# Kernel tuning notes

Measured on AMD Instinct MI355X. Metric: run time of the kernel, lower is better.

Reference implementation:

```python
import jax, jax.numpy as jnp
import numpy as np

WIRES = 4
DIM = 16  # 2**WIRES
EPS = 1e-5


def _rot_matrix(phi, theta, omega):
    # PennyLane Rot = RZ(omega) RY(theta) RZ(phi)
    c = jnp.cos(theta / 2).astype(jnp.complex64)
    s = jnp.sin(theta / 2).astype(jnp.complex64)
    ep = jnp.exp(-0.5j * (phi + omega).astype(jnp.complex64))
    em = jnp.exp(0.5j * (phi - omega).astype(jnp.complex64))
    m00 = ep * c
    m01 = -em * s
    m10 = jnp.conj(em) * s
    m11 = jnp.conj(ep) * c
    return jnp.stack([jnp.stack([m00, m01]), jnp.stack([m10, m11])])


def _apply_1q(state4, U, w):
    # state4: (B,2,2,2,2); apply 2x2 unitary on wire w (axis w+1)
    st = jnp.moveaxis(state4, w + 1, -1)
    st = st @ U.T  # sum_j st[...,j] * U[i,j]
    return jnp.moveaxis(st, -1, w + 1)


def _cnot_perm(c, t):
    # permutation of 16 basis indices for CNOT(control=c, target=t); wire 0 = MSB
    idx = np.arange(DIM)
    cbit = (idx >> (WIRES - 1 - c)) & 1
    return idx ^ (cbit << (WIRES - 1 - t))


def _circuit(x16, params):
    # AmplitudeEmbedding with normalize=True
    B = x16.shape[0]
    nrm = jnp.linalg.norm(x16, axis=1, keepdims=True)
    state = (x16 / nrm).astype(jnp.complex64)  # (B,16)
    L = params.shape[0]
    for l in range(L):
        st4 = state.reshape(B, 2, 2, 2, 2)
        for w in range(WIRES):
            U = _rot_matrix(params[l, w, 0], params[l, w, 1], params[l, w, 2])
            st4 = _apply_1q(st4, U, w)
        state = st4.reshape(B, DIM)
        r = (l % (WIRES - 1)) + 1  # StronglyEntanglingLayers default range
        for w in range(WIRES):
            perm = _cnot_perm(w, (w + r) % WIRES)
            state = state[:, perm]
    probs = (state.real ** 2 + state.imag ** 2)  # (B,16)
    p4 = probs.reshape(B, 2, 2, 2, 2)
    # <Z_w> = P(bit_w=0) - P(bit_w=1)
    outs = []
    for w in range(WIRES):
        axes = tuple(a for a in range(1, 5) if a != w + 1)
        pw = p4.sum(axis=axes)  # (B,2)
        outs.append(pw[:, 0] - pw[:, 1])
    return jnp.stack(outs, axis=1)  # (B,4)


def setup_inputs() -> dict:
    key = jax.random.key(0)
    k1, k2 = jax.random.split(key)
    B = 65536
    x = jax.random.normal(k1, (B, 1, 24, 24), dtype=jnp.float32)
    params = jax.random.normal(k2, (2, WIRES, 3), dtype=jnp.float32)
    gamma = jnp.ones((WIRES,), dtype=jnp.float32)
    beta = jnp.zeros((WIRES,), dtype=jnp.float32)
    return {"x": x, "params": params, "gamma": gamma, "beta": beta}


def reference(x, params, gamma, beta):
    B = x.shape[0]
    # avg_pool2d kernel 6: (B,1,24,24) -> (B,1,4,4) -> (B,16)
    pooled = x.reshape(B, 1, 4, 6, 4, 6).mean(axis=(3, 5)).reshape(B, DIM)
    out = _circuit(pooled, params)  # (B,4)
    # BatchNorm1d in training mode (biased batch stats)
    mu = out.mean(axis=0)
    var = ((out - mu) ** 2).mean(axis=0)
    return (out - mu) / jnp.sqrt(var + EPS) * gamma + beta
```

## Files before the change

kernel.cpp:

```cpp
#include <hip/hip_runtime.h>
#include <math.h>

#define BATCH 65536
#define XPER  576
#define NBLK  1024
#define WPB   4
#define RPW   2
#define IPR   8


__global__ __launch_bounds__(256, 3) void circuit_kernel(
        const float* __restrict__ x, const float* __restrict__ params,
        float* __restrict__ out, float* __restrict__ slots) {
    __shared__ float sUr[16 * 20];
    __shared__ float sUi[16 * 20];
    __shared__ float sg[48];
    __shared__ float sv[WPB][IPR * 20];
    __shared__ float spart[8];

    const int t    = threadIdx.x;
    const int wid  = t >> 6;
    const int lane = t & 63;
    const int e    = lane >> 3;
    const int q    = lane & 7;
    const int pr   = q >> 1;
    const int P    = q & 1;

    if (t < 8) {
        spart[t] = 0.0f;
        float phi   = params[t * 3 + 0];
        float theta = params[t * 3 + 1];
        float omega = params[t * 3 + 2];
        float apo = 0.5f * (phi + omega), amo = 0.5f * (phi - omega);
        sg[t * 6 + 0] = cosf(0.5f * theta);
        sg[t * 6 + 1] = sinf(0.5f * theta);
        sg[t * 6 + 2] = cosf(apo);
        sg[t * 6 + 3] = -sinf(apo);
        sg[t * 6 + 4] = cosf(amo);
        sg[t * 6 + 5] = sinf(amo);
    }
    __syncthreads();

    if (t < 16) {
        const int j = t;
        float Mr[16], Mi[16];
#pragma unroll
        for (int i = 0; i < 16; ++i) { Mr[i] = (i == j) ? 1.0f : 0.0f; Mi[i] = 0.0f; }
#pragma unroll
        for (int l = 0; l < 2; ++l) {
#pragma unroll
            for (int w = 0; w < 4; ++w) {
                const int g = l * 4 + w;
                float c   = sg[g * 6 + 0], s   = sg[g * 6 + 1];
                float epr = sg[g * 6 + 2], epi = sg[g * 6 + 3];
                float emr = sg[g * 6 + 4], emi = sg[g * 6 + 5];
                float m00r =  epr * c, m00i =  epi * c;
                float m01r = -emr * s, m01i = -emi * s;
                float m10r =  emr * s, m10i = -emi * s;
                float m11r =  epr * c, m11i = -epi * c;
                const int mask = 1 << (3 - w);
#pragma unroll
                for (int i = 0; i < 16; ++i) {
                    if (i & mask) continue;
                    int i1 = i | mask;
                    float r0 = Mr[i],  q0 = Mi[i];
                    float r1 = Mr[i1], q1 = Mi[i1];
                    Mr[i]  = m00r * r0 - m00i * q0 + m01r * r1 - m01i * q1;
                    Mi[i]  = m00r * q0 + m00i * r0 + m01r * q1 + m01i * r1;
                    Mr[i1] = m10r * r0 - m10i * q0 + m11r * r1 - m11i * q1;
                    Mi[i1] = m10r * q0 + m10i * r0 + m11r * q1 + m11i * r1;
                }
            }
            const int rr = (l % 3) + 1;
#pragma unroll
            for (int w = 0; w < 4; ++w) {
                int tq = (w + rr) & 3;
                int cb = 3 - w, tb = 3 - tq;
#pragma unroll
                for (int i = 0; i < 16; ++i) {
                    int pi = i ^ (((i >> cb) & 1) << tb);
                    if (pi > i) {
                        float tr = Mr[i]; Mr[i] = Mr[pi]; Mr[pi] = tr;
                        float ti = Mi[i]; Mi[i] = Mi[pi]; Mi[pi] = ti;
                    }
                }
            }
        }
#pragma unroll
        for (int i = 0; i < 16; ++i) {
            sUr[i * 20 + j] = Mr[i];
            sUi[i * 20 + j] = Mi[i];
        }
    }
    __syncthreads();

    float u0r[16], u0i[16], u1r[16], u1i[16];
    {
        const float4* r0 = (const float4*)(sUr + (2 * q) * 20);
        const float4* r1 = (const float4*)(sUr + (2 * q + 1) * 20);
        const float4* i0 = (const float4*)(sUi + (2 * q) * 20);
        const float4* i1 = (const float4*)(sUi + (2 * q + 1) * 20);
#pragma unroll
        for (int m = 0; m < 4; ++m) {
            float4 a = r0[m], b = r1[m], cc = i0[m], d = i1[m];
            u0r[4*m+0]=a.x; u0r[4*m+1]=a.y; u0r[4*m+2]=a.z; u0r[4*m+3]=a.w;
            u1r[4*m+0]=b.x; u1r[4*m+1]=b.y; u1r[4*m+2]=b.z; u1r[4*m+3]=b.w;
            u0i[4*m+0]=cc.x; u0i[4*m+1]=cc.y; u0i[4*m+2]=cc.z; u0i[4*m+3]=cc.w;
            u1i[4*m+0]=d.x; u1i[4*m+1]=d.y; u1i[4*m+2]=d.z; u1i[4*m+3]=d.w;
        }
    }

    int c = -1;
    if      (q == 4) c = 0;
    else if (q == 2) c = 1;
    else if (q == 1) c = 2;
    else if (q == 0) c = 3;

    const int cbase = pr * 144 + P * 12;
    float accz = 0.0f, accz2 = 0.0f;

#pragma unroll
    for (int rd = 0; rd < RPW; ++rd) {
        const size_t img = (size_t)blockIdx.x * 64 + wid * 16 + rd * 8 + e;
        const float* ip = x + img * XPER + cbase;

        float L = 0.0f, R = 0.0f;
#pragma unroll
        for (int r = 0; r < 6; ++r) {
            float4 a = *(const float4*)(ip + r * 24);
            float4 b = *(const float4*)(ip + r * 24 + 4);
            float4 d = *(const float4*)(ip + r * 24 + 8);
            L += a.x + a.y + a.z + a.w + b.x + b.y;
            R += b.z + b.w + d.x + d.y + d.z + d.w;
        }
        float vL = L * (1.0f / 36.0f), vR = R * (1.0f / 36.0f);

        *(float2*)(&sv[wid][e * 20 + 2 * q]) = make_float2(vL, vR);
        float vv[16];
        {
            const float4* vb = (const float4*)(&sv[wid][e * 20]);
#pragma unroll
            for (int m = 0; m < 4; ++m) {
                float4 a = vb[m];
                vv[4*m+0]=a.x; vv[4*m+1]=a.y; vv[4*m+2]=a.z; vv[4*m+3]=a.w;
            }
        }

        float n2 = 0.0f, sr0 = 0.0f, si0 = 0.0f, sr1 = 0.0f, si1 = 0.0f;
#pragma unroll
        for (int j = 0; j < 16; ++j) {
            float vj = vv[j];
            n2  = fmaf(vj, vj, n2);
            sr0 = fmaf(u0r[j], vj, sr0); si0 = fmaf(u0i[j], vj, si0);
            sr1 = fmaf(u1r[j], vj, sr1); si1 = fmaf(u1i[j], vj, si1);
        }
        float inv = 1.0f / n2;
        float p0 = (sr0 * sr0 + si0 * si0) * inv;
        float p1 = (sr1 * sr1 + si1 * si1) * inv;

        float u = p0 + p1, d = p0 - p1, o;
        o = __shfl_xor(u, 1); u = (q & 1) ? (o - u) : (u + o);
        o = __shfl_xor(u, 2); u = (q & 2) ? (o - u) : (u + o);
        o = __shfl_xor(u, 4); u = (q & 4) ? (o - u) : (u + o);
        d += __shfl_xor(d, 1);
        d += __shfl_xor(d, 2);
        d += __shfl_xor(d, 4);

        if (c >= 0) {
            float z = (q == 0) ? d : u;
            out[img * 4 + c] = z;
            accz  += z;
            accz2 += z * z;
        }
    }

    if (c >= 0) {
        atomicAdd(&spart[c], accz);
        atomicAdd(&spart[4 + c], accz2);
    }
    __syncthreads();
    if (t < 8) slots[blockIdx.x * 8 + t] = spart[t];
}

__global__ __launch_bounds__(256) void bn_apply(float* __restrict__ out,
                                                const float* __restrict__ slots,
                                                const float* __restrict__ gamma,
                                                const float* __restrict__ beta) {
    __shared__ float red[256];
    __shared__ float sc[8];
    const int t = threadIdx.x;
    const int ch = t & 7, g = t >> 3;
    float s = 0.0f;
#pragma unroll
    for (int k = 0; k < NBLK / 32; ++k)
        s += slots[(size_t)(g + 32 * k) * 8 + ch];
    red[t] = s;
    __syncthreads();
#pragma unroll
    for (int stp = 128; stp >= 8; stp >>= 1) {
        if (t < stp) red[t] += red[t + stp];
        __syncthreads();
    }
    if (t < 4) {
        float mu  = red[t] * (1.0f / BATCH);
        float var = red[4 + t] * (1.0f / BATCH) - mu * mu;
        float a = gamma[t] * rsqrtf(var + 1e-5f);
        sc[t]     = a;
        sc[4 + t] = beta[t] - mu * a;
    }
    __syncthreads();
    int i = blockIdx.x * 256 + t;
    float4 z = ((float4*)out)[i];
    z.x = fmaf(z.x, sc[0], sc[4]);
    z.y = fmaf(z.y, sc[1], sc[5]);
    z.z = fmaf(z.z, sc[2], sc[6]);
    z.w = fmaf(z.w, sc[3], sc[7]);
    ((float4*)out)[i] = z;
}

extern "C" void kernel_launch(void* const* d_in, const int* in_sizes, int n_in,
                              void* d_out, int out_size, void* d_ws, size_t ws_size,
                              hipStream_t stream) {
    const float* x      = (const float*)d_in[0];
    const float* params = (const float*)d_in[1];
    const float* gamma  = (const float*)d_in[2];
    const float* beta   = (const float*)d_in[3];
    float* out = (float*)d_out;
    float* ws  = (float*)d_ws;

    hipLaunchKernelGGL(circuit_kernel, dim3(NBLK), dim3(256), 0, stream,
                       x, params, out, ws);
    hipLaunchKernelGGL(bn_apply, dim3(BATCH / 256), dim3(256), 0, stream,
                       out, ws, gamma, beta);
}
```

Before: 36.05 us.

## Coalesce image loads across wave and pool via LDS atomics

Each wave now reads its eight images as one contiguous block, with each lane loading consecutive float4s, instead of each lane walking strided rows of its own 6x12 patch. The pooling partial sums are scattered into per-wave LDS accumulators with atomicAdd, using precomputed per-lane bin indices. The unitary rows are read from LDS inside the dot-product loop rather than kept in registers, and the four outputs per image are gathered by shuffle into a single float4 store. The aim is better global-load coalescing and lower register pressure, at the cost of many LDS atomics and extra LDS traffic. The occupancy hint in launch bounds is also dropped.

```diff
diff --git a/kernel.cpp b/kernel.cpp
--- a/kernel.cpp
+++ b/kernel.cpp
@@ -9,13 +9,13 @@
 #define IPR   8
 
 
-__global__ __launch_bounds__(256, 3) void circuit_kernel(
+__global__ __launch_bounds__(256) void circuit_kernel(
         const float* __restrict__ x, const float* __restrict__ params,
         float* __restrict__ out, float* __restrict__ slots) {
     __shared__ float sUr[16 * 20];
     __shared__ float sUi[16 * 20];
     __shared__ float sg[48];
-    __shared__ float sv[WPB][IPR * 20];
+    __shared__ float sacc[WPB][160];
     __shared__ float spart[8];
 
     const int t    = threadIdx.x;
@@ -23,8 +23,6 @@
     const int lane = t & 63;
     const int e    = lane >> 3;
     const int q    = lane & 7;
-    const int pr   = q >> 1;
-    const int P    = q & 1;
 
     if (t < 8) {
         spart[t] = 0.0f;
@@ -94,21 +92,20 @@
     }
     __syncthreads();
 
-    float u0r[16], u0i[16], u1r[16], u1i[16];
-    {
-        const float4* r0 = (const float4*)(sUr + (2 * q) * 20);
-        const float4* r1 = (const float4*)(sUr + (2 * q + 1) * 20);
-        const float4* i0 = (const float4*)(sUi + (2 * q) * 20);
-        const float4* i1 = (const float4*)(sUi + (2 * q + 1) * 20);
-#pragma unroll
-        for (int m = 0; m < 4; ++m) {
-            float4 a = r0[m], b = r1[m], cc = i0[m], d = i1[m];
-            u0r[4*m+0]=a.x; u0r[4*m+1]=a.y; u0r[4*m+2]=a.z; u0r[4*m+3]=a.w;
-            u1r[4*m+0]=b.x; u1r[4*m+1]=b.y; u1r[4*m+2]=b.z; u1r[4*m+3]=b.w;
-            u0i[4*m+0]=cc.x; u0i[4*m+1]=cc.y; u0i[4*m+2]=cc.z; u0i[4*m+3]=cc.w;
-            u1i[4*m+0]=d.x; u1i[4*m+1]=d.y; u1i[4*m+2]=d.z; u1i[4*m+3]=d.w;
-        }
-    }
+    int accIdx[18];
+    unsigned spMask = 0;
+#pragma unroll
+    for (int j = 0; j < 18; ++j) {
+        int fidx = j * 256 + lane * 4;
+        int img  = fidx / 576;
+        int rem  = fidx - img * 576;
+        int row  = rem / 24;
+        int col  = rem - row * 24;
+        int cc   = col / 6;
+        accIdx[j] = img * 16 + (row / 6) * 4 + cc;
+        if (col - cc * 6 == 4) spMask |= (1u << j);
+    }
+    float* const accBase = &sacc[wid][0];
 
     int c = -1;
     if      (q == 4) c = 0;
@@ -116,43 +113,49 @@
     else if (q == 1) c = 2;
     else if (q == 0) c = 3;
 
-    const int cbase = pr * 144 + P * 12;
     float accz = 0.0f, accz2 = 0.0f;
+    const size_t blockImg = (size_t)blockIdx.x * (WPB * RPW * IPR);
 
 #pragma unroll
     for (int rd = 0; rd < RPW; ++rd) {
-        const size_t img = (size_t)blockIdx.x * 64 + wid * 16 + rd * 8 + e;
-        const float* ip = x + img * XPER + cbase;
-
-        float L = 0.0f, R = 0.0f;
-#pragma unroll
-        for (int r = 0; r < 6; ++r) {
-            float4 a = *(const float4*)(ip + r * 24);
-            float4 b = *(const float4*)(ip + r * 24 + 4);
-            float4 d = *(const float4*)(ip + r * 24 + 8);
-            L += a.x + a.y + a.z + a.w + b.x + b.y;
-            R += b.z + b.w + d.x + d.y + d.z + d.w;
-        }
-        float vL = L * (1.0f / 36.0f), vR = R * (1.0f / 36.0f);
-
-        *(float2*)(&sv[wid][e * 20 + 2 * q]) = make_float2(vL, vR);
-        float vv[16];
-        {
-            const float4* vb = (const float4*)(&sv[wid][e * 20]);
-#pragma unroll
-            for (int m = 0; m < 4; ++m) {
-                float4 a = vb[m];
-                vv[4*m+0]=a.x; vv[4*m+1]=a.y; vv[4*m+2]=a.z; vv[4*m+3]=a.w;
+        const size_t img0 = blockImg + (size_t)wid * (RPW * IPR) + (size_t)rd * IPR;
+        const float* cb = x + img0 * XPER;
+
+        accBase[lane]      = 0.0f;
+        accBase[lane + 64] = 0.0f;
+
+#pragma unroll
+        for (int b = 0; b < 2; ++b) {
+            float4 r[9];
+#pragma unroll
+            for (int j2 = 0; j2 < 9; ++j2)
+                r[j2] = *(const float4*)(cb + (b * 9 + j2) * 256 + lane * 4);
+#pragma unroll
+            for (int j2 = 0; j2 < 9; ++j2) {
+                const int j = b * 9 + j2;
+                float s01 = r[j2].x + r[j2].y;
+                float s23 = r[j2].z + r[j2].w;
+                bool  sp  = (spMask >> j) & 1;
+                float sA  = sp ? s01 : (s01 + s23);
+                atomicAdd(accBase + accIdx[j], sA);
+                if (sp) atomicAdd(accBase + accIdx[j] + 1, s23);
             }
         }
+        __builtin_amdgcn_sched_barrier(0);
 
         float n2 = 0.0f, sr0 = 0.0f, si0 = 0.0f, sr1 = 0.0f, si1 = 0.0f;
 #pragma unroll
-        for (int j = 0; j < 16; ++j) {
-            float vj = vv[j];
-            n2  = fmaf(vj, vj, n2);
-            sr0 = fmaf(u0r[j], vj, sr0); si0 = fmaf(u0i[j], vj, si0);
-            sr1 = fmaf(u1r[j], vj, sr1); si1 = fmaf(u1i[j], vj, si1);
+        for (int m = 0; m < 4; ++m) {
+            float4 v4 = *(const float4*)(accBase + e * 16 + 4 * m);
+            float4 a0 = *(const float4*)(sUr + (2 * q) * 20 + 4 * m);
+            float4 b0 = *(const float4*)(sUi + (2 * q) * 20 + 4 * m);
+            float4 a1 = *(const float4*)(sUr + (2 * q + 1) * 20 + 4 * m);
+            float4 b1 = *(const float4*)(sUi + (2 * q + 1) * 20 + 4 * m);
+            n2  = fmaf(v4.x, v4.x, fmaf(v4.y, v4.y, fmaf(v4.z, v4.z, fmaf(v4.w, v4.w, n2))));
+            sr0 = fmaf(a0.x, v4.x, fmaf(a0.y, v4.y, fmaf(a0.z, v4.z, fmaf(a0.w, v4.w, sr0))));
+            si0 = fmaf(b0.x, v4.x, fmaf(b0.y, v4.y, fmaf(b0.z, v4.z, fmaf(b0.w, v4.w, si0))));
+            sr1 = fmaf(a1.x, v4.x, fmaf(a1.y, v4.y, fmaf(a1.z, v4.z, fmaf(a1.w, v4.w, sr1))));
+            si1 = fmaf(b1.x, v4.x, fmaf(b1.y, v4.y, fmaf(b1.z, v4.z, fmaf(b1.w, v4.w, si1))));
         }
         float inv = 1.0f / n2;
         float p0 = (sr0 * sr0 + si0 * si0) * inv;
@@ -166,12 +169,15 @@
         d += __shfl_xor(d, 2);
         d += __shfl_xor(d, 4);
 
-        if (c >= 0) {
-            float z = (q == 0) ? d : u;
-            out[img * 4 + c] = z;
-            accz  += z;
-            accz2 += z * z;
-        }
+        float z = (q == 0) ? d : u;
+        if (c >= 0) { accz += z; accz2 += z * z; }
+
+        int gb = lane & ~7;
+        float z0 = __shfl(z, gb | 4);
+        float z1 = __shfl(z, gb | 2);
+        float z2 = __shfl(z, gb | 1);
+        if (q == 0)
+            ((float4*)out)[img0 + e] = make_float4(z0, z1, z2, z);
     }
 
     if (c >= 0) {
```

New measurement: 84.87 us. 135% more time.

## Process one image per wave slot, double grid, read unitary from LDS, vectorize output store

Applied to the files above, without the earlier changes.

Each block now handles 32 images instead of 64 (one round per wave instead of two), with the grid doubled to 2048 blocks and the min-waves launch bound removed. The 64 per-thread unitary registers are replaced by float4 LDS reads inside the matvec loop, cutting register pressure. Output is gathered via shuffles so one lane writes a float4 per image instead of four scalar stores. The trade-off is more blocks, each redoing the per-block unitary construction, plus extra LDS traffic and twice as many partial-sum slots for the batch-norm kernel to reduce.

```diff
diff --git a/kernel.cpp b/kernel.cpp
--- a/kernel.cpp
+++ b/kernel.cpp
@@ -3,13 +3,12 @@
 
 #define BATCH 65536
 #define XPER  576
-#define NBLK  1024
+#define NBLK  2048
 #define WPB   4
-#define RPW   2
 #define IPR   8
 
 
-__global__ __launch_bounds__(256, 3) void circuit_kernel(
+__global__ __launch_bounds__(256) void circuit_kernel(
         const float* __restrict__ x, const float* __restrict__ params,
         float* __restrict__ out, float* __restrict__ slots) {
     __shared__ float sUr[16 * 20];
@@ -94,22 +93,6 @@
     }
     __syncthreads();
 
-    float u0r[16], u0i[16], u1r[16], u1i[16];
-    {
-        const float4* r0 = (const float4*)(sUr + (2 * q) * 20);
-        const float4* r1 = (const float4*)(sUr + (2 * q + 1) * 20);
-        const float4* i0 = (const float4*)(sUi + (2 * q) * 20);
-        const float4* i1 = (const float4*)(sUi + (2 * q + 1) * 20);
-#pragma unroll
-        for (int m = 0; m < 4; ++m) {
-            float4 a = r0[m], b = r1[m], cc = i0[m], d = i1[m];
-            u0r[4*m+0]=a.x; u0r[4*m+1]=a.y; u0r[4*m+2]=a.z; u0r[4*m+3]=a.w;
-            u1r[4*m+0]=b.x; u1r[4*m+1]=b.y; u1r[4*m+2]=b.z; u1r[4*m+3]=b.w;
-            u0i[4*m+0]=cc.x; u0i[4*m+1]=cc.y; u0i[4*m+2]=cc.z; u0i[4*m+3]=cc.w;
-            u1i[4*m+0]=d.x; u1i[4*m+1]=d.y; u1i[4*m+2]=d.z; u1i[4*m+3]=d.w;
-        }
-    }
-
     int c = -1;
     if      (q == 4) c = 0;
     else if (q == 2) c = 1;
@@ -117,66 +100,61 @@
     else if (q == 0) c = 3;
 
     const int cbase = pr * 144 + P * 12;
-    float accz = 0.0f, accz2 = 0.0f;
-
-#pragma unroll
-    for (int rd = 0; rd < RPW; ++rd) {
-        const size_t img = (size_t)blockIdx.x * 64 + wid * 16 + rd * 8 + e;
-        const float* ip = x + img * XPER + cbase;
-
-        float L = 0.0f, R = 0.0f;
-#pragma unroll
-        for (int r = 0; r < 6; ++r) {
-            float4 a = *(const float4*)(ip + r * 24);
-            float4 b = *(const float4*)(ip + r * 24 + 4);
-            float4 d = *(const float4*)(ip + r * 24 + 8);
-            L += a.x + a.y + a.z + a.w + b.x + b.y;
-            R += b.z + b.w + d.x + d.y + d.z + d.w;
-        }
-        float vL = L * (1.0f / 36.0f), vR = R * (1.0f / 36.0f);
-
-        *(float2*)(&sv[wid][e * 20 + 2 * q]) = make_float2(vL, vR);
-        float vv[16];
-        {
-            const float4* vb = (const float4*)(&sv[wid][e * 20]);
-#pragma unroll
-            for (int m = 0; m < 4; ++m) {
-                float4 a = vb[m];
-                vv[4*m+0]=a.x; vv[4*m+1]=a.y; vv[4*m+2]=a.z; vv[4*m+3]=a.w;
-            }
-        }
-
-        float n2 = 0.0f, sr0 = 0.0f, si0 = 0.0f, sr1 = 0.0f, si1 = 0.0f;
-#pragma unroll
-        for (int j = 0; j < 16; ++j) {
-            float vj = vv[j];
-            n2  = fmaf(vj, vj, n2);
-            sr0 = fmaf(u0r[j], vj, sr0); si0 = fmaf(u0i[j], vj, si0);
-            sr1 = fmaf(u1r[j], vj, sr1); si1 = fmaf(u1i[j], vj, si1);
-        }
-        float inv = 1.0f / n2;
-        float p0 = (sr0 * sr0 + si0 * si0) * inv;
-        float p1 = (sr1 * sr1 + si1 * si1) * inv;
-
-        float u = p0 + p1, d = p0 - p1, o;
-        o = __shfl_xor(u, 1); u = (q & 1) ? (o - u) : (u + o);
-        o = __shfl_xor(u, 2); u = (q & 2) ? (o - u) : (u + o);
-        o = __shfl_xor(u, 4); u = (q & 4) ? (o - u) : (u + o);
-        d += __shfl_xor(d, 1);
-        d += __shfl_xor(d, 2);
-        d += __shfl_xor(d, 4);
-
-        if (c >= 0) {
-            float z = (q == 0) ? d : u;
-            out[img * 4 + c] = z;
-            accz  += z;
-            accz2 += z * z;
-        }
-    }
+    const size_t img0 = (size_t)blockIdx.x * 32 + (size_t)wid * IPR;
+    const size_t img  = img0 + e;
+    const float* ip = x + img * XPER + cbase;
+
+    float L = 0.0f, R = 0.0f;
+#pragma unroll
+    for (int r = 0; r < 6; ++r) {
+        float4 a = *(const float4*)(ip + r * 24);
+        float4 b = *(const float4*)(ip + r * 24 + 4);
+        float4 d = *(const float4*)(ip + r * 24 + 8);
+        L += a.x + a.y + a.z + a.w + b.x + b.y;
+        R += b.z + b.w + d.x + d.y + d.z + d.w;
+    }
+    float vL = L * (1.0f / 36.0f), vR = R * (1.0f / 36.0f);
+
+    *(float2*)(&sv[wid][e * 20 + 2 * q]) = make_float2(vL, vR);
+
+    float n2 = 0.0f, sr0 = 0.0f, si0 = 0.0f, sr1 = 0.0f, si1 = 0.0f;
+#pragma unroll
+    for (int m = 0; m < 4; ++m) {
+        float4 v4 = *(const float4*)(&sv[wid][e * 20 + 4 * m]);
+        float4 a0 = *(const float4*)(sUr + (2 * q) * 20 + 4 * m);
+        float4 b0 = *(const float4*)(sUi + (2 * q) * 20 + 4 * m);
+        float4 a1 = *(const float4*)(sUr + (2 * q + 1) * 20 + 4 * m);
+        float4 b1 = *(const float4*)(sUi + (2 * q + 1) * 20 + 4 * m);
+        n2  = fmaf(v4.x, v4.x, fmaf(v4.y, v4.y, fmaf(v4.z, v4.z, fmaf(v4.w, v4.w, n2))));
+        sr0 = fmaf(a0.x, v4.x, fmaf(a0.y, v4.y, fmaf(a0.z, v4.z, fmaf(a0.w, v4.w, sr0))));
+        si0 = fmaf(b0.x, v4.x, fmaf(b0.y, v4.y, fmaf(b0.z, v4.z, fmaf(b0.w, v4.w, si0))));
+        sr1 = fmaf(a1.x, v4.x, fmaf(a1.y, v4.y, fmaf(a1.z, v4.z, fmaf(a1.w, v4.w, sr1))));
+        si1 = fmaf(b1.x, v4.x, fmaf(b1.y, v4.y, fmaf(b1.z, v4.z, fmaf(b1.w, v4.w, si1))));
+    }
+    float inv = 1.0f / n2;
+    float p0 = (sr0 * sr0 + si0 * si0) * inv;
+    float p1 = (sr1 * sr1 + si1 * si1) * inv;
+
+    float u = p0 + p1, d = p0 - p1, o;
+    o = __shfl_xor(u, 1); u = (q & 1) ? (o - u) : (u + o);
+    o = __shfl_xor(u, 2); u = (q & 2) ? (o - u) : (u + o);
+    o = __shfl_xor(u, 4); u = (q & 4) ? (o - u) : (u + o);
+    d += __shfl_xor(d, 1);
+    d += __shfl_xor(d, 2);
+    d += __shfl_xor(d, 4);
+
+    float z = (q == 0) ? d : u;
+
+    int gb = lane & ~7;
+    float z0 = __shfl(z, gb | 4);
+    float z1 = __shfl(z, gb | 2);
+    float z2 = __shfl(z, gb | 1);
+    if (q == 0)
+        ((float4*)out)[img] = make_float4(z0, z1, z2, z);
 
     if (c >= 0) {
-        atomicAdd(&spart[c], accz);
-        atomicAdd(&spart[4 + c], accz2);
+        atomicAdd(&spart[c], z);
+        atomicAdd(&spart[4 + c], z * z);
     }
     __syncthreads();
     if (t < 8) slots[blockIdx.x * 8 + t] = spart[t];
```

Result: no change. 36.23 us (+0.5%).
